# Kernel tuning notes

Measured on AMD Instinct MI355X. Metric: run time of the kernel, lower is better.

## Reference

```python
import jax, jax.numpy as jnp
import numpy as np

N_NODES = 50000
N_EDGES = 800000
F_IN = 128          # num_features
F_HID = 128 * 3     # conv1 out
F_OUT = 256         # num_relations = num_criteria**2
N_CRIT = 16         # num_criteria


def setup_inputs() -> dict:
    key = jax.random.key(0)
    k_feat, k_edge, k_w1, k_w2 = jax.random.split(key, 4)
    features = jax.random.normal(k_feat, (N_NODES, F_IN), dtype=jnp.float32)
    edge_index = jax.random.randint(k_edge, (2, N_EDGES), 0, N_NODES, dtype=jnp.int32)
    # Glorot-ish init like dglnn.GraphConv
    W1 = jax.random.normal(k_w1, (F_IN, F_HID), dtype=jnp.float32) * (1.0 / np.sqrt(F_IN))
    b1 = jnp.zeros((F_HID,), dtype=jnp.float32)
    W2 = jax.random.normal(k_w2, (F_HID, F_OUT), dtype=jnp.float32) * (1.0 / np.sqrt(F_HID))
    b2 = jnp.zeros((F_OUT,), dtype=jnp.float32)
    return {"features": features, "W1": W1, "b1": b1, "W2": W2, "b2": b2,
            "edge_index": edge_index}


def reference(features, W1, b1, W2, b2, edge_index):
    src, dst = edge_index[0], edge_index[1]
    ones = jnp.ones((edge_index.shape[1],), dtype=features.dtype)
    # symmetric GCN norm with degrees clamped to min 1 (DGL norm='both')
    deg_out = jax.ops.segment_sum(ones, src, num_segments=N_NODES)
    deg_in = jax.ops.segment_sum(ones, dst, num_segments=N_NODES)
    out_norm = jnp.clip(deg_out, 1.0, None) ** -0.5   # [N]
    in_norm = jnp.clip(deg_in, 1.0, None) ** -0.5     # [N]

    def aggregate(h):
        # h: [N, d] -> D_in^{-1/2} A D_out^{-1/2} h  via edge gather + segment_sum
        msg = (h * out_norm[:, None])[src]                              # [E, d]
        return jax.ops.segment_sum(msg, dst, num_segments=N_NODES) * in_norm[:, None]

    # conv1: in(128) < out(384) -> aggregate first, then dense transform
    x = jax.nn.relu(aggregate(features) @ W1 + b1)      # [N, 384]
    # conv2: in(384) > out(256) -> dense transform first, then aggregate
    x = aggregate(x @ W2) + b2                          # [N, 256]
    return x.reshape(-1, N_CRIT, N_CRIT)                # [N, 16, 16]
```

## Files before the change

kernel.cpp:

```cpp
#include <hip/hip_runtime.h>
#include <hip/hip_bf16.h>

typedef float f32x4 __attribute__((ext_vector_type(4)));
typedef __bf16 bf16x8 __attribute__((ext_vector_type(8)));

#define NNODES 50000
#define NEDGES 800000
#define FIN 128
#define FHID 384
#define FOUT 256

#define SCAN_NB ((NNODES + 1023) / 1024)

#define HB 128
#define EPB (NEDGES / HB)
#define HW (NNODES / 2)

__device__ __forceinline__ float bf_lo(unsigned u) { return __uint_as_float(u << 16); }
__device__ __forceinline__ float bf_hi(unsigned u) { return __uint_as_float(u & 0xffff0000u); }
__device__ __forceinline__ unsigned short f2bf(float f) {
  unsigned u = __float_as_uint(f);
  u += 0x7fffu + ((u >> 16) & 1u);
  return (unsigned short)(u >> 16);
}

__global__ void cvt_feat_kernel(const float* __restrict__ f,
                                const float* __restrict__ onorm,
                                unsigned short* __restrict__ o, int n4) {
  int i = blockIdx.x * blockDim.x + threadIdx.x;
  if (i >= n4) return;
  float4 v = *(const float4*)(f + (size_t)i * 4);
  float w = onorm[(i * 4) >> 7];
  ushort4 r;
  r.x = f2bf(v.x * w); r.y = f2bf(v.y * w);
  r.z = f2bf(v.z * w); r.w = f2bf(v.w * w);
  *(ushort4*)(o + (size_t)i * 4) = r;
}

__global__ void wt_both(const float* __restrict__ W1, const float* __restrict__ W2,
                        __bf16* __restrict__ W1t, __bf16* __restrict__ W2t) {
  int i = blockIdx.x * blockDim.x + threadIdx.x;
  if (i < FIN * FHID) {
    int k = i / FHID, n = i % FHID;
    unsigned short b = f2bf(W1[i]);
    W1t[(size_t)n * FIN + k] = *(__bf16*)&b;
  } else if (i < FIN * FHID + FHID * FOUT) {
    int j = i - FIN * FHID;
    int k = j / FOUT, n = j % FOUT;
    unsigned short b = f2bf(W2[j]);
    W2t[(size_t)n * FHID + k] = *(__bf16*)&b;
  }
}

__global__ __launch_bounds__(1024) void hist_kernel(
    const int* __restrict__ ei, unsigned* __restrict__ psrc,
    unsigned* __restrict__ pdst, unsigned short* __restrict__ rank) {
  __shared__ unsigned hist[HW];
  int b = blockIdx.x, pass = blockIdx.y, t = threadIdx.x;
  for (int i = t; i < HW; i += 1024) hist[i] = 0;
  __syncthreads();
  const int* idx = ei + (pass ? NEDGES : 0) + b * EPB;
  if (pass == 0) {
    for (int i = t; i < EPB; i += 1024) {
      int n = idx[i];
      atomicAdd(&hist[n >> 1], 1u << ((n & 1) << 4));
    }
  } else {
    for (int i = t; i < EPB; i += 1024) {
      int n = idx[i];
      unsigned sh = (n & 1) << 4;
      unsigned old = atomicAdd(&hist[n >> 1], 1u << sh);
      rank[b * EPB + i] = (unsigned short)((old >> sh) & 0xFFFFu);
    }
  }
  __syncthreads();
  unsigned* dst = (pass ? pdst : psrc) + (size_t)b * HW;
  for (int i = t; i < HW; i += 1024) dst[i] = hist[i];
}

__global__ __launch_bounds__(256) void reduce_hist(
    const unsigned* __restrict__ psrc, unsigned* __restrict__ pdst,
    int* __restrict__ din, float* __restrict__ onorm, float* __restrict__ inorm) {
  int w = blockIdx.x * blockDim.x + threadIdx.x;
  if (w >= HW) return;
  unsigned sl = 0, sh = 0;
#pragma unroll 8
  for (int b = 0; b < HB; ++b) {
    unsigned v = psrc[(size_t)b * HW + w];
    sl += v & 0xFFFFu; sh += v >> 16;
  }
  unsigned rl = 0, rh = 0;
#pragma unroll 8
  for (int b = 0; b < HB; ++b) {
    size_t o = (size_t)b * HW + w;
    unsigned v = pdst[o];
    pdst[o] = rl | (rh << 16);
    rl += v & 0xFFFFu; rh += v >> 16;
  }
  int n0 = 2 * w, n1 = 2 * w + 1;
  din[n0] = (int)rl; din[n1] = (int)rh;
  onorm[n0] = rsqrtf((float)(sl ? sl : 1u));
  onorm[n1] = rsqrtf((float)(sh ? sh : 1u));
  inorm[n0] = rsqrtf((float)(rl ? rl : 1u));
  inorm[n1] = rsqrtf((float)(rh ? rh : 1u));
}

__global__ __launch_bounds__(256) void scan_part1(const int* __restrict__ deg,
                                                  int* __restrict__ blocksums) {
  int b = blockIdx.x, t = threadIdx.x;
  int base = b * 1024 + t * 4;
  int s = 0;
  if (base + 4 <= NNODES) {
    int4 v = *(const int4*)(deg + base);
    s = v.x + v.y + v.z + v.w;
  } else {
    for (int j = 0; j < 4; ++j)
      if (base + j < NNODES) s += deg[base + j];
  }
  for (int d = 32; d >= 1; d >>= 1) s += __shfl_down(s, d, 64);
  __shared__ int ws[4];
  int lane = t & 63, w = t >> 6;
  if (lane == 0) ws[w] = s;
  __syncthreads();
  if (t == 0) blocksums[b] = ws[0] + ws[1] + ws[2] + ws[3];
}

__global__ void scan_mid(const int* __restrict__ bs, int* __restrict__ boff) {
  int t = threadIdx.x;
  int v = (t < SCAN_NB) ? bs[t] : 0;
  int x = v;
  for (int d = 1; d < 64; d <<= 1) {
    int y = __shfl_up(x, d, 64);
    if (t >= d) x += y;
  }
  if (t < SCAN_NB) boff[t] = x - v;
}

__global__ __launch_bounds__(256) void scan_part2(const int* __restrict__ deg,
                                                  const int* __restrict__ boff,
                                                  int* __restrict__ row_ptr) {
  int b = blockIdx.x, t = threadIdx.x;
  int base = b * 1024 + t * 4;
  int v0 = 0, v1 = 0, v2 = 0, v3 = 0;
  if (base + 4 <= NNODES) {
    int4 v = *(const int4*)(deg + base);
    v0 = v.x; v1 = v.y; v2 = v.z; v3 = v.w;
  } else {
    if (base + 0 < NNODES) v0 = deg[base + 0];
    if (base + 1 < NNODES) v1 = deg[base + 1];
    if (base + 2 < NNODES) v2 = deg[base + 2];
    if (base + 3 < NNODES) v3 = deg[base + 3];
  }
  int s = v0 + v1 + v2 + v3;
  int x = s;
  int lane = t & 63, w = t >> 6;
  for (int d = 1; d < 64; d <<= 1) {
    int y = __shfl_up(x, d, 64);
    if (lane >= d) x += y;
  }
  __shared__ int ws[4];
  if (lane == 63) ws[w] = x;
  __syncthreads();
  int woff = 0;
  for (int i = 0; i < w; ++i) woff += ws[i];
  int off = boff[b] + woff + (x - s);
  if (base + 0 < NNODES) { row_ptr[base + 0] = off; off += v0; }
  if (base + 1 < NNODES) { row_ptr[base + 1] = off; off += v1; }
  if (base + 2 < NNODES) { row_ptr[base + 2] = off; off += v2; }
  if (base + 3 < NNODES) { row_ptr[base + 3] = off; off += v3; }
  if (base < NNODES && base + 4 >= NNODES) row_ptr[NNODES] = off;
}

__global__ void fill_kernel(const int* __restrict__ ei,
                            const unsigned short* __restrict__ rank,
                            const unsigned* __restrict__ pdst,
                            const int* __restrict__ row_ptr,
                            int* __restrict__ csr) {
  int e = blockIdx.x * blockDim.x + threadIdx.x;
  if (e >= NEDGES) return;
  int n = ei[NEDGES + e];
  int b = e / EPB;
  unsigned base = (pdst[(size_t)b * HW + (n >> 1)] >> ((n & 1) << 4)) & 0xFFFFu;
  csr[row_ptr[n] + (int)base + (int)rank[e]] = ei[e];
}

__global__ __launch_bounds__(256) void agg1_kernel(
    const int* __restrict__ row_ptr, const int* __restrict__ csr,
    const float* __restrict__ inorm, const unsigned short* __restrict__ featb,
    unsigned short* __restrict__ aggF) {
  int node = (blockIdx.x << 2) + (threadIdx.x >> 6);
  if (node >= NNODES) return;
  int lane = threadIdx.x & 63;
  int quarter = lane >> 4;
  int fl8 = (lane & 15) << 3;
  const unsigned short* tab = featb + fl8;
  int beg = row_ptr[node], end = row_ptr[node + 1];
  float a0 = 0.f, a1 = 0.f, a2 = 0.f, a3 = 0.f, a4 = 0.f, a5 = 0.f, a6 = 0.f, a7 = 0.f;
  int e = beg;
  for (; e + 16 <= end; e += 16) {
    int s0 = __builtin_nontemporal_load(&csr[e + quarter]);
    int s1 = __builtin_nontemporal_load(&csr[e + 4 + quarter]);
    int s2 = __builtin_nontemporal_load(&csr[e + 8 + quarter]);
    int s3 = __builtin_nontemporal_load(&csr[e + 12 + quarter]);
    uint4 v0 = *(const uint4*)(tab + (size_t)s0 * FIN);
    uint4 v1 = *(const uint4*)(tab + (size_t)s1 * FIN);
    uint4 v2 = *(const uint4*)(tab + (size_t)s2 * FIN);
    uint4 v3 = *(const uint4*)(tab + (size_t)s3 * FIN);
    a0 += bf_lo(v0.x); a1 += bf_hi(v0.x); a2 += bf_lo(v0.y); a3 += bf_hi(v0.y);
    a4 += bf_lo(v0.z); a5 += bf_hi(v0.z); a6 += bf_lo(v0.w); a7 += bf_hi(v0.w);
    a0 += bf_lo(v1.x); a1 += bf_hi(v1.x); a2 += bf_lo(v1.y); a3 += bf_hi(v1.y);
    a4 += bf_lo(v1.z); a5 += bf_hi(v1.z); a6 += bf_lo(v1.w); a7 += bf_hi(v1.w);
    a0 += bf_lo(v2.x); a1 += bf_hi(v2.x); a2 += bf_lo(v2.y); a3 += bf_hi(v2.y);
    a4 += bf_lo(v2.z); a5 += bf_hi(v2.z); a6 += bf_lo(v2.w); a7 += bf_hi(v2.w);
    a0 += bf_lo(v3.x); a1 += bf_hi(v3.x); a2 += bf_lo(v3.y); a3 += bf_hi(v3.y);
    a4 += bf_lo(v3.z); a5 += bf_hi(v3.z); a6 += bf_lo(v3.w); a7 += bf_hi(v3.w);
  }
  if (e + 8 <= end) {
    int s0 = __builtin_nontemporal_load(&csr[e + quarter]);
    int s1 = __builtin_nontemporal_load(&csr[e + 4 + quarter]);
    uint4 v0 = *(const uint4*)(tab + (size_t)s0 * FIN);
    uint4 v1 = *(const uint4*)(tab + (size_t)s1 * FIN);
    a0 += bf_lo(v0.x); a1 += bf_hi(v0.x); a2 += bf_lo(v0.y); a3 += bf_hi(v0.y);
    a4 += bf_lo(v0.z); a5 += bf_hi(v0.z); a6 += bf_lo(v0.w); a7 += bf_hi(v0.w);
    a0 += bf_lo(v1.x); a1 += bf_hi(v1.x); a2 += bf_lo(v1.y); a3 += bf_hi(v1.y);
    a4 += bf_lo(v1.z); a5 += bf_hi(v1.z); a6 += bf_lo(v1.w); a7 += bf_hi(v1.w);
    e += 8;
  }
  for (int t = e + quarter; t < end; t += 4) {
    int s0 = __builtin_nontemporal_load(&csr[t]);
    uint4 v0 = *(const uint4*)(tab + (size_t)s0 * FIN);
    a0 += bf_lo(v0.x); a1 += bf_hi(v0.x); a2 += bf_lo(v0.y); a3 += bf_hi(v0.y);
    a4 += bf_lo(v0.z); a5 += bf_hi(v0.z); a6 += bf_lo(v0.w); a7 += bf_hi(v0.w);
  }
  a0 += __shfl_xor(a0, 16, 64); a1 += __shfl_xor(a1, 16, 64);
  a2 += __shfl_xor(a2, 16, 64); a3 += __shfl_xor(a3, 16, 64);
  a4 += __shfl_xor(a4, 16, 64); a5 += __shfl_xor(a5, 16, 64);
  a6 += __shfl_xor(a6, 16, 64); a7 += __shfl_xor(a7, 16, 64);
  a0 += __shfl_xor(a0, 32, 64); a1 += __shfl_xor(a1, 32, 64);
  a2 += __shfl_xor(a2, 32, 64); a3 += __shfl_xor(a3, 32, 64);
  a4 += __shfl_xor(a4, 32, 64); a5 += __shfl_xor(a5, 32, 64);
  a6 += __shfl_xor(a6, 32, 64); a7 += __shfl_xor(a7, 32, 64);
  float p0 = (quarter == 0) ? a0 : (quarter == 1) ? a2 : (quarter == 2) ? a4 : a6;
  float p1 = (quarter == 0) ? a1 : (quarter == 1) ? a3 : (quarter == 2) ? a5 : a7;
  float inn = inorm[node];
  unsigned pk = (unsigned)f2bf(p0 * inn) | ((unsigned)f2bf(p1 * inn) << 16);
  *(unsigned*)(aggF + (size_t)node * FIN + fl8 + (quarter << 1)) = pk;
}

__global__ __launch_bounds__(256) void agg2_kernel(
    const int* __restrict__ row_ptr, const int* __restrict__ csr,
    const float* __restrict__ inorm, const unsigned short* __restrict__ h2s,
    const float* __restrict__ b2, float* __restrict__ out) {
  int node = (blockIdx.x << 2) + (threadIdx.x >> 6);
  if (node >= NNODES) return;
  int lane = threadIdx.x & 63;
  int half = lane >> 5;
  int fl8 = (lane & 31) << 3;
  const unsigned short* tab = h2s + fl8;
  int beg = row_ptr[node], end = row_ptr[node + 1];
  float a0 = 0.f, a1 = 0.f, a2 = 0.f, a3 = 0.f, a4 = 0.f, a5 = 0.f, a6 = 0.f, a7 = 0.f;
  int e = beg;
  for (; e + 8 <= end; e += 8) {
    int s0 = __builtin_nontemporal_load(&csr[e + half]);
    int s1 = __builtin_nontemporal_load(&csr[e + 2 + half]);
    int s2 = __builtin_nontemporal_load(&csr[e + 4 + half]);
    int s3 = __builtin_nontemporal_load(&csr[e + 6 + half]);
    uint4 v0 = *(const uint4*)(tab + (size_t)s0 * FOUT);
    uint4 v1 = *(const uint4*)(tab + (size_t)s1 * FOUT);
    uint4 v2 = *(const uint4*)(tab + (size_t)s2 * FOUT);
    uint4 v3 = *(const uint4*)(tab + (size_t)s3 * FOUT);
    a0 += bf_lo(v0.x); a1 += bf_hi(v0.x); a2 += bf_lo(v0.y); a3 += bf_hi(v0.y);
    a4 += bf_lo(v0.z); a5 += bf_hi(v0.z); a6 += bf_lo(v0.w); a7 += bf_hi(v0.w);
    a0 += bf_lo(v1.x); a1 += bf_hi(v1.x); a2 += bf_lo(v1.y); a3 += bf_hi(v1.y);
    a4 += bf_lo(v1.z); a5 += bf_hi(v1.z); a6 += bf_lo(v1.w); a7 += bf_hi(v1.w);
    a0 += bf_lo(v2.x); a1 += bf_hi(v2.x); a2 += bf_lo(v2.y); a3 += bf_hi(v2.y);
    a4 += bf_lo(v2.z); a5 += bf_hi(v2.z); a6 += bf_lo(v2.w); a7 += bf_hi(v2.w);
    a0 += bf_lo(v3.x); a1 += bf_hi(v3.x); a2 += bf_lo(v3.y); a3 += bf_hi(v3.y);
    a4 += bf_lo(v3.z); a5 += bf_hi(v3.z); a6 += bf_lo(v3.w); a7 += bf_hi(v3.w);
  }
  if (e + 4 <= end) {
    int s0 = __builtin_nontemporal_load(&csr[e + half]);
    int s1 = __builtin_nontemporal_load(&csr[e + 2 + half]);
    uint4 v0 = *(const uint4*)(tab + (size_t)s0 * FOUT);
    uint4 v1 = *(const uint4*)(tab + (size_t)s1 * FOUT);
    a0 += bf_lo(v0.x); a1 += bf_hi(v0.x); a2 += bf_lo(v0.y); a3 += bf_hi(v0.y);
    a4 += bf_lo(v0.z); a5 += bf_hi(v0.z); a6 += bf_lo(v0.w); a7 += bf_hi(v0.w);
    a0 += bf_lo(v1.x); a1 += bf_hi(v1.x); a2 += bf_lo(v1.y); a3 += bf_hi(v1.y);
    a4 += bf_lo(v1.z); a5 += bf_hi(v1.z); a6 += bf_lo(v1.w); a7 += bf_hi(v1.w);
    e += 4;
  }
  for (int t = e + half; t < end; t += 2) {
    int s0 = __builtin_nontemporal_load(&csr[t]);
    uint4 v0 = *(const uint4*)(tab + (size_t)s0 * FOUT);
    a0 += bf_lo(v0.x); a1 += bf_hi(v0.x); a2 += bf_lo(v0.y); a3 += bf_hi(v0.y);
    a4 += bf_lo(v0.z); a5 += bf_hi(v0.z); a6 += bf_lo(v0.w); a7 += bf_hi(v0.w);
  }
  a0 += __shfl_xor(a0, 32, 64); a1 += __shfl_xor(a1, 32, 64);
  a2 += __shfl_xor(a2, 32, 64); a3 += __shfl_xor(a3, 32, 64);
  a4 += __shfl_xor(a4, 32, 64); a5 += __shfl_xor(a5, 32, 64);
  a6 += __shfl_xor(a6, 32, 64); a7 += __shfl_xor(a7, 32, 64);
  float q0 = half ? a4 : a0;
  float q1 = half ? a5 : a1;
  float q2 = half ? a6 : a2;
  float q3 = half ? a7 : a3;
  int f = fl8 + (half << 2);
  float inn = inorm[node];
  float4 bv = *(const float4*)(b2 + f);
  f32x4 r;
  r.x = fmaf(q0, inn, bv.x);
  r.y = fmaf(q1, inn, bv.y);
  r.z = fmaf(q2, inn, bv.z);
  r.w = fmaf(q3, inn, bv.w);
  __builtin_nontemporal_store(r, (f32x4*)(out + (size_t)node * FOUT + f));
}

__device__ __forceinline__ f32x4 mfma16(bf16x8 a, bf16x8 b, f32x4 c) {
  return __builtin_amdgcn_mfma_f32_16x16x32_bf16(a, b, c, 0, 0, 0);
}

__global__ __launch_bounds__(256) void gemm_bf16(
    const __bf16* __restrict__ A, const __bf16* __restrict__ Bt,
    const float* __restrict__ bias, const float* __restrict__ row_scale,
    __bf16* __restrict__ C, int M, int N, int K, int relu) {
  __shared__ __attribute__((aligned(16))) __bf16 As[128 * 64];
  __shared__ __attribute__((aligned(16))) __bf16 Bs[128 * 64];
  const int tid = threadIdx.x;
  const int lane = tid & 63;
  const int wave = tid >> 6;
  const int wm = (wave >> 1) << 6;
  const int wn = (wave & 1) << 6;
  const int r16 = lane & 15;
  const int kg = lane >> 4;
  const int m0 = blockIdx.x * 128;
  const int n0 = blockIdx.y * 128;
  f32x4 acc[4][4];
#pragma unroll
  for (int m = 0; m < 4; ++m)
#pragma unroll
    for (int n = 0; n < 4; ++n) acc[m][n] = f32x4{0.f, 0.f, 0.f, 0.f};

  for (int k0 = 0; k0 < K; k0 += 64) {
    __syncthreads();
#pragma unroll
    for (int i = 0; i < 4; ++i) {
      int c = tid + (i << 8);
      int row = c >> 3;
      int col = c & 7;
      int sw = ((col ^ (row & 7)) << 3);
      int ga = m0 + row;
      uint4 av = make_uint4(0u, 0u, 0u, 0u);
      if (ga < M) av = *(const uint4*)(A + (size_t)ga * K + k0 + (col << 3));
      *(uint4*)(As + row * 64 + sw) = av;
      uint4 bv = *(const uint4*)(Bt + (size_t)(n0 + row) * K + k0 + (col << 3));
      *(uint4*)(Bs + row * 64 + sw) = bv;
    }
    __syncthreads();
#pragma unroll
    for (int kk = 0; kk < 2; ++kk) {
      int kc = (kk << 2) + kg;
      bf16x8 a[4], b[4];
#pragma unroll
      for (int m = 0; m < 4; ++m) {
        int r = wm + (m << 4) + r16;
        a[m] = *(const bf16x8*)(As + r * 64 + ((kc ^ (r & 7)) << 3));
      }
#pragma unroll
      for (int n = 0; n < 4; ++n) {
        int r = wn + (n << 4) + r16;
        b[n] = *(const bf16x8*)(Bs + r * 64 + ((kc ^ (r & 7)) << 3));
      }
#pragma unroll
      for (int m = 0; m < 4; ++m)
#pragma unroll
        for (int n = 0; n < 4; ++n)
          acc[m][n] = mfma16(a[m], b[n], acc[m][n]);
    }
  }
#pragma unroll
  for (int m = 0; m < 4; ++m) {
#pragma unroll
    for (int j = 0; j < 4; ++j) {
      int row = m0 + wm + (m << 4) + (kg << 2) + j;
      if (row < M) {
        float sc = row_scale ? row_scale[row] : 1.f;
#pragma unroll
        for (int n = 0; n < 4; ++n) {
          int col = n0 + wn + (n << 4) + r16;
          float v = acc[m][n][j] + (bias ? bias[col] : 0.f);
          if (relu) v = fmaxf(v, 0.f);
          v *= sc;
          unsigned short h = f2bf(v);
          C[(size_t)row * N + col] = *(__bf16*)&h;
        }
      }
    }
  }
}

extern "C" void kernel_launch(void* const* d_in, const int* in_sizes, int n_in,
                              void* d_out, int out_size, void* d_ws, size_t ws_size,
                              hipStream_t stream) {
  const float* features = (const float*)d_in[0];
  const float* W1 = (const float*)d_in[1];
  const float* b1 = (const float*)d_in[2];
  const float* W2 = (const float*)d_in[3];
  const float* b2 = (const float*)d_in[4];
  const int* ei = (const int*)d_in[5];
  float* out = (float*)d_out;

  char* ws = (char*)d_ws;
  size_t off = 0;
  auto alloc = [&](size_t bytes) -> void* {
    void* p = ws + off;
    off += (bytes + 255) & ~(size_t)255;
    return p;
  };
  float* onorm  = (float*)alloc((size_t)NNODES * 4);
  float* inorm  = (float*)alloc((size_t)NNODES * 4);
  int* din      = (int*)alloc((size_t)NNODES * 4);
  int* row_ptr  = (int*)alloc((size_t)(NNODES + 1) * 4);
  int* csr_src  = (int*)alloc((size_t)NEDGES * 4);
  int* blocksums = (int*)alloc((size_t)SCAN_NB * 4);
  int* blockoffs = (int*)alloc((size_t)SCAN_NB * 4);
  unsigned short* featb = (unsigned short*)alloc((size_t)NNODES * FIN * 2);
  unsigned short* aggF  = (unsigned short*)alloc((size_t)NNODES * FIN * 2);
  __bf16* h1  = (__bf16*)alloc((size_t)NNODES * FHID * 2);
  __bf16* h2s = (__bf16*)alloc((size_t)NNODES * FOUT * 2);
  __bf16* W1t = (__bf16*)alloc((size_t)FIN * FHID * 2);
  __bf16* W2t = (__bf16*)alloc((size_t)FHID * FOUT * 2);
  (void)ws_size; (void)n_in; (void)in_sizes; (void)out_size;

  unsigned* psrc = (unsigned*)h1;
  unsigned* pdst = psrc + (size_t)HB * HW;
  unsigned short* rank = (unsigned short*)(pdst + (size_t)HB * HW);

  hist_kernel<<<dim3(HB, 2), 1024, 0, stream>>>(ei, psrc, pdst, rank);
  reduce_hist<<<(HW + 255) / 256, 256, 0, stream>>>(psrc, pdst, din, onorm, inorm);
  scan_part1<<<SCAN_NB, 256, 0, stream>>>(din, blocksums);
  scan_mid<<<1, 64, 0, stream>>>(blocksums, blockoffs);
  scan_part2<<<SCAN_NB, 256, 0, stream>>>(din, blockoffs, row_ptr);
  fill_kernel<<<(NEDGES + 255) / 256, 256, 0, stream>>>(ei, rank, pdst, row_ptr, csr_src);

  cvt_feat_kernel<<<(NNODES * FIN / 4 + 255) / 256, 256, 0, stream>>>(
      features, onorm, featb, NNODES * FIN / 4);
  wt_both<<<(FIN * FHID + FHID * FOUT + 255) / 256, 256, 0, stream>>>(W1, W2, W1t, W2t);

  agg1_kernel<<<(NNODES + 3) / 4, 256, 0, stream>>>(
      row_ptr, csr_src, inorm, featb, aggF);
  gemm_bf16<<<dim3((NNODES + 127) / 128, FHID / 128), 256, 0, stream>>>(
      (const __bf16*)aggF, W1t, b1, nullptr, h1, NNODES, FHID, FIN, 1);

  gemm_bf16<<<dim3((NNODES + 127) / 128, FOUT / 128), 256, 0, stream>>>(
      h1, W2t, nullptr, onorm, h2s, NNODES, FOUT, FHID, 0);
  agg2_kernel<<<(NNODES + 3) / 4, 256, 0, stream>>>(
      row_ptr, csr_src, inorm, (const unsigned short*)h2s, b2, out);
}
```

Before: 310.3 us.

## Keep A row-panel resident in LDS and loop over all N panels per block

```diff
diff --git a/kernel.cpp b/kernel.cpp
--- a/kernel.cpp
+++ b/kernel.cpp
@@ -318,11 +318,12 @@
   return __builtin_amdgcn_mfma_f32_16x16x32_bf16(a, b, c, 0, 0, 0);
 }
 
-__global__ __launch_bounds__(256) void gemm_bf16(
+template<int K, int NPANELS>
+__global__ __launch_bounds__(256) void gemm_ar(
     const __bf16* __restrict__ A, const __bf16* __restrict__ Bt,
     const float* __restrict__ bias, const float* __restrict__ row_scale,
-    __bf16* __restrict__ C, int M, int N, int K, int relu) {
-  __shared__ __attribute__((aligned(16))) __bf16 As[128 * 64];
+    __bf16* __restrict__ C, int M, int N, int relu) {
+  __shared__ __attribute__((aligned(16))) __bf16 As[128 * K];
   __shared__ __attribute__((aligned(16))) __bf16 Bs[128 * 64];
   const int tid = threadIdx.x;
   const int lane = tid & 63;
@@ -332,65 +333,82 @@
   const int r16 = lane & 15;
   const int kg = lane >> 4;
   const int m0 = blockIdx.x * 128;
-  const int n0 = blockIdx.y * 128;
-  f32x4 acc[4][4];
-#pragma unroll
-  for (int m = 0; m < 4; ++m)
-#pragma unroll
-    for (int n = 0; n < 4; ++n) acc[m][n] = f32x4{0.f, 0.f, 0.f, 0.f};
-
-  for (int k0 = 0; k0 < K; k0 += 64) {
-    __syncthreads();
+
+#pragma unroll
+  for (int c = 0; c < K / 64; ++c) {
+    __bf16* Ac = As + c * (128 * 64);
 #pragma unroll
     for (int i = 0; i < 4; ++i) {
-      int c = tid + (i << 8);
-      int row = c >> 3;
-      int col = c & 7;
+      int ch = tid + (i << 8);
+      int row = ch >> 3;
+      int col = ch & 7;
       int sw = ((col ^ (row & 7)) << 3);
       int ga = m0 + row;
       uint4 av = make_uint4(0u, 0u, 0u, 0u);
-      if (ga < M) av = *(const uint4*)(A + (size_t)ga * K + k0 + (col << 3));
-      *(uint4*)(As + row * 64 + sw) = av;
-      uint4 bv = *(const uint4*)(Bt + (size_t)(n0 + row) * K + k0 + (col << 3));
-      *(uint4*)(Bs + row * 64 + sw) = bv;
+      if (ga < M) av = *(const uint4*)(A + (size_t)ga * K + c * 64 + (col << 3));
+      *(uint4*)(Ac + row * 64 + sw) = av;
     }
-    __syncthreads();
-#pragma unroll
-    for (int kk = 0; kk < 2; ++kk) {
-      int kc = (kk << 2) + kg;
-      bf16x8 a[4], b[4];
-#pragma unroll
-      for (int m = 0; m < 4; ++m) {
-        int r = wm + (m << 4) + r16;
-        a[m] = *(const bf16x8*)(As + r * 64 + ((kc ^ (r & 7)) << 3));
+  }
+
+  for (int p = 0; p < NPANELS; ++p) {
+    const int n0 = p * 128;
+    f32x4 acc[4][4];
+#pragma unroll
+    for (int m = 0; m < 4; ++m)
+#pragma unroll
+      for (int n = 0; n < 4; ++n) acc[m][n] = f32x4{0.f, 0.f, 0.f, 0.f};
+
+#pragma unroll
+    for (int c = 0; c < K / 64; ++c) {
+      __syncthreads();
+#pragma unroll
+      for (int i = 0; i < 4; ++i) {
+        int ch = tid + (i << 8);
+        int row = ch >> 3;
+        int col = ch & 7;
+        int sw = ((col ^ (row & 7)) << 3);
+        uint4 bv = *(const uint4*)(Bt + (size_t)(n0 + row) * K + c * 64 + (col << 3));
+        *(uint4*)(Bs + row * 64 + sw) = bv;
       }
-#pragma unroll
-      for (int n = 0; n < 4; ++n) {
-        int r = wn + (n << 4) + r16;
-        b[n] = *(const bf16x8*)(Bs + r * 64 + ((kc ^ (r & 7)) << 3));
+      __syncthreads();
+      const __bf16* Ac = As + c * (128 * 64);
+#pragma unroll
+      for (int kk = 0; kk < 2; ++kk) {
+        int kc = (kk << 2) + kg;
+        bf16x8 a[4], b[4];
+#pragma unroll
+        for (int m = 0; m < 4; ++m) {
+          int r = wm + (m << 4) + r16;
+          a[m] = *(const bf16x8*)(Ac + r * 64 + ((kc ^ (r & 7)) << 3));
+        }
+#pragma unroll
+        for (int n = 0; n < 4; ++n) {
+          int r = wn + (n << 4) + r16;
+          b[n] = *(const bf16x8*)(Bs + r * 64 + ((kc ^ (r & 7)) << 3));
+        }
+#pragma unroll
+        for (int m = 0; m < 4; ++m)
+#pragma unroll
+          for (int n = 0; n < 4; ++n)
+            acc[m][n] = mfma16(a[m], b[n], acc[m][n]);
       }
-#pragma unroll
-      for (int m = 0; m < 4; ++m)
-#pragma unroll
-        for (int n = 0; n < 4; ++n)
-          acc[m][n] = mfma16(a[m], b[n], acc[m][n]);
     }
-  }
-#pragma unroll
-  for (int m = 0; m < 4; ++m) {
-#pragma unroll
-    for (int j = 0; j < 4; ++j) {
-      int row = m0 + wm + (m << 4) + (kg << 2) + j;
-      if (row < M) {
-        float sc = row_scale ? row_scale[row] : 1.f;
-#pragma unroll
-        for (int n = 0; n < 4; ++n) {
-          int col = n0 + wn + (n << 4) + r16;
-          float v = acc[m][n][j] + (bias ? bias[col] : 0.f);
-          if (relu) v = fmaxf(v, 0.f);
-          v *= sc;
-          unsigned short h = f2bf(v);
-          C[(size_t)row * N + col] = *(__bf16*)&h;
+#pragma unroll
+    for (int m = 0; m < 4; ++m) {
+#pragma unroll
+      for (int j = 0; j < 4; ++j) {
+        int row = m0 + wm + (m << 4) + (kg << 2) + j;
+        if (row < M) {
+          float sc = row_scale ? row_scale[row] : 1.f;
+#pragma unroll
+          for (int n = 0; n < 4; ++n) {
+            int col = n0 + wn + (n << 4) + r16;
+            float v = acc[m][n][j] + (bias ? bias[col] : 0.f);
+            if (relu) v = fmaxf(v, 0.f);
+            v *= sc;
+            unsigned short h = f2bf(v);
+            C[(size_t)row * N + col] = *(__bf16*)&h;
+          }
         }
       }
     }
@@ -447,11 +465,11 @@
 
   agg1_kernel<<<(NNODES + 3) / 4, 256, 0, stream>>>(
       row_ptr, csr_src, inorm, featb, aggF);
-  gemm_bf16<<<dim3((NNODES + 127) / 128, FHID / 128), 256, 0, stream>>>(
-      (const __bf16*)aggF, W1t, b1, nullptr, h1, NNODES, FHID, FIN, 1);
-
-  gemm_bf16<<<dim3((NNODES + 127) / 128, FOUT / 128), 256, 0, stream>>>(
-      h1, W2t, nullptr, onorm, h2s, NNODES, FOUT, FHID, 0);
+  gemm_ar<FIN, FHID / 128><<<(NNODES + 127) / 128, 256, 0, stream>>>(
+      (const __bf16*)aggF, W1t, b1, nullptr, h1, NNODES, FHID, 1);
+
+  gemm_ar<FHID, FOUT / 128><<<(NNODES + 127) / 128, 256, 0, stream>>>(
+      h1, W2t, nullptr, onorm, h2s, NNODES, FOUT, 0);
   agg2_kernel<<<(NNODES + 3) / 4, 256, 0, stream>>>(
       row_ptr, csr_src, inorm, (const unsigned short*)h2s, b2, out);
 }
```

Measured after the change: 340.3 us. +9.7%, slower.
